# Optimization experiments

Hardware: AMD Instinct MI355X
Metric: run time of the kernel (lower is better)

The kernel has to match this reference:

```python
import jax, jax.numpy as jnp
import numpy as np

B, C, L = 4, 256, 2048
HEADS, DIM_HEAD = 8, 64
HIDDEN = HEADS * DIM_HEAD  # 512


def setup_inputs() -> dict:
    key = jax.random.key(0)
    k1, k2, k3, k4 = jax.random.split(key, 4)
    x = jax.random.normal(k1, (B, C, L), dtype=jnp.float32)
    # Conv1d kernel_size=1 weights, squeezed to [out_ch, in_ch]
    w_qkv = jax.random.normal(k2, (3 * HIDDEN, C), dtype=jnp.float32) * (1.0 / np.sqrt(C))
    w_out = jax.random.normal(k3, (C, HIDDEN), dtype=jnp.float32) * (1.0 / np.sqrt(HIDDEN))
    b_out = jax.random.normal(k4, (C,), dtype=jnp.float32) * 0.01
    return {"x": x, "w_qkv": w_qkv, "w_out": w_out, "b_out": b_out}


def reference(x, w_qkv, w_out, b_out):
    b, c, l = x.shape
    scale = DIM_HEAD ** (-0.5)
    # pointwise conv == channel matmul
    qkv = jnp.einsum('oc,bcl->bol', w_qkv, x)  # [b, 3*hidden, l]
    q, k, v = jnp.split(qkv, 3, axis=1)        # each [b, hidden, l]
    def to_heads(t):
        return t.reshape(b, HEADS, DIM_HEAD, l)  # b h d l
    q, k, v = to_heads(q), to_heads(k), to_heads(v)
    q = q * scale
    sim = jnp.einsum('bhdi,bhdj->bhij', q, k)   # [b,h,l,l]
    attn = jax.nn.softmax(sim, axis=-1)          # stable softmax (max-subtract inside)
    out = jnp.einsum('bhij,bhdj->bhid', attn, v)  # [b,h,l,d]
    out = out.transpose(0, 1, 3, 2).reshape(b, HIDDEN, l)  # b (h d) l
    return jnp.einsum('oc,bcl->bol', w_out, out) + b_out[None, :, None]
```

## Files before the change

### kernel.cpp

```cpp
#include <hip/hip_runtime.h>

typedef unsigned short u16;
typedef __bf16 bf16x8 __attribute__((ext_vector_type(8)));
typedef float f32x4 __attribute__((ext_vector_type(4)));

#define MFMA16(a, b, c) __builtin_amdgcn_mfma_f32_16x16x32_bf16((a), (b), (c), 0, 0, 0)

#define Bn 4
#define Cn 256
#define Ln 2048
#define Hn 8
#define Dn 64
#define HID 512

__device__ __forceinline__ u16 bf16_rne(float f) {
  unsigned u = __builtin_bit_cast(unsigned, f);
  u += 0x7FFFu + ((u >> 16) & 1u);
  return (u16)(u >> 16);
}

__device__ __forceinline__ float fast_exp2(float x) {
#if __has_builtin(__builtin_amdgcn_exp2f)
  return __builtin_amdgcn_exp2f(x);
#else
  return exp2f(x);
#endif
}

__device__ __forceinline__ float fast_rcp(float x) {
#if __has_builtin(__builtin_amdgcn_rcpf)
  return __builtin_amdgcn_rcpf(x);
#else
  return 1.0f / x;
#endif
}

__device__ __forceinline__ void async_load16(const u16* g, u16* l) {
  __builtin_amdgcn_global_load_lds(
      (const __attribute__((address_space(1))) void*)g,
      (__attribute__((address_space(3))) void*)l, 16, 0, 0);
}

__global__ __launch_bounds__(256) void prep_weights(const float* __restrict__ wqkv,
                                                    const float* __restrict__ wout,
                                                    u16* __restrict__ wq,
                                                    u16* __restrict__ wo) {
  int i = blockIdx.x * 256 + threadIdx.x;
  const float QSCALE = 0.125f * 1.44269504088896340736f;
  if (i < 3 * HID * Cn) {
    float v = wqkv[i];
    if (i < HID * Cn) v *= QSCALE;
    wq[i] = bf16_rne(v);
  } else {
    int j = i - 3 * HID * Cn;
    wo[j] = bf16_rne(wout[j]);
  }
}

__global__ __launch_bounds__(256) void transpose_x(const float* __restrict__ x,
                                                   u16* __restrict__ xT) {
  __shared__ u16 tile[64][72];
  const int b = blockIdx.z, ct = blockIdx.y, lt = blockIdx.x;
  const int t = threadIdx.x;
  const float* xp = x + ((size_t)b * Cn + ct * 64) * Ln + lt * 64;
  for (int pass = 0; pass < 4; ++pass) {
    int c = pass * 16 + (t >> 4);
    int l4 = (t & 15) * 4;
    float4 v = *(const float4*)(xp + (size_t)c * Ln + l4);
    tile[l4 + 0][c] = bf16_rne(v.x);
    tile[l4 + 1][c] = bf16_rne(v.y);
    tile[l4 + 2][c] = bf16_rne(v.z);
    tile[l4 + 3][c] = bf16_rne(v.w);
  }
  __syncthreads();
  u16* op = xT + ((size_t)b * Ln + lt * 64) * Cn + ct * 64;
  for (int pass = 0; pass < 2; ++pass) {
    int id = pass * 256 + t;
    int l = id >> 3, c8 = (id & 7) * 8;
    *(uint4*)(op + (size_t)l * Cn + c8) = *(const uint4*)&tile[l][c8];
  }
}

__global__ __launch_bounds__(256) void qkv_gemm(const u16* __restrict__ wq,
                                                const u16* __restrict__ xT,
                                                u16* __restrict__ qT,
                                                u16* __restrict__ kT,
                                                u16* __restrict__ vv) {
  __shared__ u16 As[4096];
  __shared__ u16 Bs[4096];
  const int t = threadIdx.x;
  const int nt = blockIdx.x, mt = blockIdx.y, b = blockIdx.z;
  const int m0 = mt * 64, n0 = nt * 64;
  const int w = t >> 6, lane = t & 63, q = lane >> 4, ln = lane & 15;

  const u16* Ag = wq + (size_t)m0 * Cn;
  const u16* Bg = xT + ((size_t)b * Ln + n0) * Cn;

  f32x4 zf = {0.f, 0.f, 0.f, 0.f};
  f32x4 acc[4];
  for (int i = 0; i < 4; ++i) acc[i] = zf;

  for (int kk = 0; kk < 4; ++kk) {
    int k0 = kk * 64;
    for (int k2 = 0; k2 < 2; ++k2) {
      int reg = k2 * 4 + w;
      int r = reg * 8 + (lane >> 3);
      int c = (lane & 7) ^ (r & 7);
      async_load16(Ag + (size_t)r * Cn + k0 + c * 8, &As[reg * 512]);
      async_load16(Bg + (size_t)r * Cn + k0 + c * 8, &Bs[reg * 512]);
    }
    __syncthreads();
    int ar = w * 16 + ln;
    bf16x8 a0 = *(const bf16x8*)&As[ar * 64 + ((q ^ (ln & 7)) * 8)];
    bf16x8 a1 = *(const bf16x8*)&As[ar * 64 + (((q + 4) ^ (ln & 7)) * 8)];
    for (int n2 = 0; n2 < 4; ++n2) {
      int br = n2 * 16 + ln;
      bf16x8 b0 = *(const bf16x8*)&Bs[br * 64 + ((q ^ (ln & 7)) * 8)];
      bf16x8 b1 = *(const bf16x8*)&Bs[br * 64 + (((q + 4) ^ (ln & 7)) * 8)];
      acc[n2] = MFMA16(a0, b0, acc[n2]);
      acc[n2] = MFMA16(a1, b1, acc[n2]);
    }
    __syncthreads();
  }
  for (int n2 = 0; n2 < 4; ++n2) {
    int l = n0 + n2 * 16 + ln;
    for (int r = 0; r < 4; ++r) {
      u16 hv = bf16_rne(acc[n2][r]);
      int od = w * 16 + q * 4 + r;
      if (mt < 8) {
        qT[(((size_t)b * Hn + mt) * Ln + l) * Dn + od] = hv;
      } else if (mt < 16) {
        kT[(((size_t)b * Hn + (mt - 8)) * Ln + l) * Dn + od] = hv;
      } else {
        int ch = (mt - 16) * 64 + od;
        vv[((size_t)b * HID + ch) * Ln + l] = hv;
      }
    }
  }
}

__global__ __launch_bounds__(256) void attention(const u16* __restrict__ qT,
                                                 const u16* __restrict__ kT,
                                                 const u16* __restrict__ vv,
                                                 u16* __restrict__ attT) {
  __shared__ u16 Kt[4096];
  __shared__ u16 Vt[4096];
  __shared__ u16 Ps[8192];
  const int t = threadIdx.x;
  const int qb = blockIdx.x, bh = blockIdx.y;
  const int b = bh >> 3, h = bh & 7;
  const int w = t >> 6, lane = t & 63, q = lane >> 4, ln = lane & 15;
  const int i0 = qb * 128 + w * 32;

  bf16x8 qa[2][2];
  for (int it = 0; it < 2; ++it) {
    const u16* qrow = qT + (((size_t)bh) * Ln + i0 + it * 16 + ln) * Dn;
    qa[it][0] = *(const bf16x8*)(qrow + q * 8);
    qa[it][1] = *(const bf16x8*)(qrow + 32 + q * 8);
  }

  const u16* ksrc0 = kT + ((size_t)bh) * Ln * Dn;
  const u16* vsrc0 = vv + ((size_t)b * HID + h * Dn) * Ln;

  bf16x8 ones;
  for (int i = 0; i < 8; ++i) ones[i] = (__bf16)1.0f;

  f32x4 zf = {0.f, 0.f, 0.f, 0.f};
  f32x4 o_acc[2][4], l_acc[2];
  for (int it = 0; it < 2; ++it) {
    l_acc[it] = zf;
    for (int d = 0; d < 4; ++d) o_acc[it][d] = zf;
  }
  u16* pw0 = Ps + w * 2048;

  for (int jt = 0; jt < 32; ++jt) {
    int j0 = jt * 64;
    for (int k2 = 0; k2 < 2; ++k2) {
      int reg = k2 * 4 + w;
      int r = reg * 8 + (lane >> 3);
      int c = (lane & 7) ^ (r & 7);
      async_load16(ksrc0 + (size_t)(j0 + r) * Dn + c * 8, &Kt[reg * 512]);
      async_load16(vsrc0 + (size_t)r * Ln + j0 + c * 8, &Vt[reg * 512]);
    }
    __syncthreads();

    f32x4 sv[2][4];
    for (int n2 = 0; n2 < 4; ++n2) {
      int jr = n2 * 16 + ln;
      bf16x8 k0f = *(const bf16x8*)&Kt[jr * 64 + ((q ^ (ln & 7)) * 8)];
      bf16x8 k1f = *(const bf16x8*)&Kt[jr * 64 + (((q + 4) ^ (ln & 7)) * 8)];
      for (int it = 0; it < 2; ++it) {
        f32x4 s = zf;
        s = MFMA16(k0f, qa[it][0], s);
        s = MFMA16(k1f, qa[it][1], s);
        sv[it][n2] = s;
      }
    }
    for (int it = 0; it < 2; ++it) {
      u16* pw = pw0 + it * 1024;
      for (int n2 = 0; n2 < 4; ++n2) {
        unsigned p01 = (unsigned)bf16_rne(fast_exp2(sv[it][n2][0])) |
                       ((unsigned)bf16_rne(fast_exp2(sv[it][n2][1])) << 16);
        unsigned p23 = (unsigned)bf16_rne(fast_exp2(sv[it][n2][2])) |
                       ((unsigned)bf16_rne(fast_exp2(sv[it][n2][3])) << 16);
        int jw = n2 * 16 + q * 4;
        int c = jw >> 3, lo = jw & 7;
        uint2 pk; pk.x = p01; pk.y = p23;
        *(uint2*)&pw[ln * 64 + ((c ^ (ln & 7)) * 8) + lo] = pk;
      }
    }
    for (int it = 0; it < 2; ++it) {
      u16* pw = pw0 + it * 1024;
      bf16x8 pa0 = *(const bf16x8*)&pw[ln * 64 + ((q ^ (ln & 7)) * 8)];
      bf16x8 pa1 = *(const bf16x8*)&pw[ln * 64 + (((q + 4) ^ (ln & 7)) * 8)];
      l_acc[it] = MFMA16(pa0, ones, l_acc[it]);
      l_acc[it] = MFMA16(pa1, ones, l_acc[it]);
      for (int d2 = 0; d2 < 4; ++d2) {
        int dr = d2 * 16 + ln;
        bf16x8 v0f = *(const bf16x8*)&Vt[dr * 64 + ((q ^ (ln & 7)) * 8)];
        bf16x8 v1f = *(const bf16x8*)&Vt[dr * 64 + (((q + 4) ^ (ln & 7)) * 8)];
        o_acc[it][d2] = MFMA16(pa0, v0f, o_acc[it][d2]);
        o_acc[it][d2] = MFMA16(pa1, v1f, o_acc[it][d2]);
      }
    }
    __syncthreads();
  }
  for (int it = 0; it < 2; ++it) {
    for (int r = 0; r < 4; ++r) {
      float rinv = fast_rcp(l_acc[it][r]);
      int i = i0 + it * 16 + q * 4 + r;
      size_t base = ((size_t)b * Ln + i) * HID + h * Dn;
      for (int d2 = 0; d2 < 4; ++d2)
        attT[base + d2 * 16 + ln] = bf16_rne(o_acc[it][d2][r] * rinv);
    }
  }
}

__global__ __launch_bounds__(256) void out_gemm(const u16* __restrict__ wo,
                                                const u16* __restrict__ attT,
                                                const float* __restrict__ bout,
                                                float* __restrict__ out) {
  __shared__ u16 As[4096];
  __shared__ u16 Bs[4096];
  const int t = threadIdx.x;
  const int nt = blockIdx.x, mt = blockIdx.y, b = blockIdx.z;
  const int m0 = mt * 64, n0 = nt * 64;
  const int w = t >> 6, lane = t & 63, q = lane >> 4, ln = lane & 15;

  const u16* Ag = wo + (size_t)m0 * HID;
  const u16* Bg = attT + ((size_t)b * Ln + n0) * HID;

  f32x4 zf = {0.f, 0.f, 0.f, 0.f};
  f32x4 acc[4];
  for (int i = 0; i < 4; ++i) acc[i] = zf;

  for (int kk = 0; kk < 8; ++kk) {
    int k0 = kk * 64;
    for (int k2 = 0; k2 < 2; ++k2) {
      int reg = k2 * 4 + w;
      int r = reg * 8 + (lane >> 3);
      int c = (lane & 7) ^ (r & 7);
      async_load16(Ag + (size_t)r * HID + k0 + c * 8, &As[reg * 512]);
      async_load16(Bg + (size_t)r * HID + k0 + c * 8, &Bs[reg * 512]);
    }
    __syncthreads();
    int ar = w * 16 + ln;
    bf16x8 a0 = *(const bf16x8*)&As[ar * 64 + ((q ^ (ln & 7)) * 8)];
    bf16x8 a1 = *(const bf16x8*)&As[ar * 64 + (((q + 4) ^ (ln & 7)) * 8)];
    for (int n2 = 0; n2 < 4; ++n2) {
      int br = n2 * 16 + ln;
      bf16x8 b0 = *(const bf16x8*)&Bs[br * 64 + ((q ^ (ln & 7)) * 8)];
      bf16x8 b1 = *(const bf16x8*)&Bs[br * 64 + (((q + 4) ^ (ln & 7)) * 8)];
      acc[n2] = MFMA16(a0, b0, acc[n2]);
      acc[n2] = MFMA16(a1, b1, acc[n2]);
    }
    __syncthreads();
  }
  float bias[4];
  for (int r = 0; r < 4; ++r) bias[r] = bout[m0 + w * 16 + q * 4 + r];
  for (int n2 = 0; n2 < 4; ++n2) {
    int l = n0 + n2 * 16 + ln;
    for (int r = 0; r < 4; ++r) {
      int o = m0 + w * 16 + q * 4 + r;
      out[((size_t)b * Cn + o) * Ln + l] = acc[n2][r] + bias[r];
    }
  }
}

extern "C" void kernel_launch(void* const* d_in, const int* in_sizes, int n_in,
                              void* d_out, int out_size, void* d_ws, size_t ws_size,
                              hipStream_t stream) {
  const float* x = (const float*)d_in[0];
  const float* wqkv = (const float*)d_in[1];
  const float* wout = (const float*)d_in[2];
  const float* bout = (const float*)d_in[3];
  float* out = (float*)d_out;
  char* ws = (char*)d_ws;

  u16* wq_b = (u16*)(ws + 0);
  u16* wo_b = (u16*)(ws + 786432);
  u16* xT   = (u16*)(ws + 1048576);
  u16* qT   = (u16*)(ws + 5242880);
  u16* kT   = (u16*)(ws + 13631488);
  u16* vv   = (u16*)(ws + 22020096);
  u16* attT = (u16*)(ws + 30408704);

  prep_weights<<<2048, 256, 0, stream>>>(wqkv, wout, wq_b, wo_b);
  transpose_x<<<dim3(32, 4, 4), 256, 0, stream>>>(x, xT);
  qkv_gemm<<<dim3(32, 24, 4), 256, 0, stream>>>(wq_b, xT, qT, kT, vv);
  attention<<<dim3(16, 32), 256, 0, stream>>>(qT, kT, vv, attT);
  out_gemm<<<dim3(32, 4, 4), 256, 0, stream>>>(wo_b, attT, bout, out);
}
```

Measured before the change: 168.9 us.

## Prefetch K/V tiles via registers and stage QKV epilogue through LDS

Measured after the change: 198.0 us. 1.17x slower.

```diff
diff --git a/kernel.cpp b/kernel.cpp
--- a/kernel.cpp
+++ b/kernel.cpp
@@ -17,6 +17,10 @@
   unsigned u = __builtin_bit_cast(unsigned, f);
   u += 0x7FFFu + ((u >> 16) & 1u);
   return (u16)(u >> 16);
+}
+
+__device__ __forceinline__ unsigned pack2(float a, float b) {
+  return (unsigned)bf16_rne(a) | ((unsigned)bf16_rne(b) << 16);
 }
 
 __device__ __forceinline__ float fast_exp2(float x) {
@@ -122,19 +126,42 @@
     }
     __syncthreads();
   }
-  for (int n2 = 0; n2 < 4; ++n2) {
-    int l = n0 + n2 * 16 + ln;
-    for (int r = 0; r < 4; ++r) {
-      u16 hv = bf16_rne(acc[n2][r]);
-      int od = w * 16 + q * 4 + r;
-      if (mt < 8) {
-        qT[(((size_t)b * Hn + mt) * Ln + l) * Dn + od] = hv;
-      } else if (mt < 16) {
-        kT[(((size_t)b * Hn + (mt - 8)) * Ln + l) * Dn + od] = hv;
-      } else {
-        int ch = (mt - 16) * 64 + od;
-        vv[((size_t)b * HID + ch) * Ln + l] = hv;
+
+  if (mt < 16) {
+    int od0 = w * 16 + q * 4;
+    int cw = od0 >> 3, lo = od0 & 7;
+    for (int n2 = 0; n2 < 4; ++n2) {
+      int l = n2 * 16 + ln;
+      uint2 pk;
+      pk.x = pack2(acc[n2][0], acc[n2][1]);
+      pk.y = pack2(acc[n2][2], acc[n2][3]);
+      *(uint2*)&As[l * 64 + ((cw ^ (l & 7)) * 8) + lo] = pk;
+    }
+    __syncthreads();
+    u16* dst = (mt < 8) ? qT + (((size_t)b * Hn + mt) * Ln + n0) * Dn
+                        : kT + (((size_t)b * Hn + (mt - 8)) * Ln + n0) * Dn;
+    for (int pass = 0; pass < 2; ++pass) {
+      int id = pass * 256 + t;
+      int l = id >> 3, c = id & 7;
+      *(uint4*)(dst + (size_t)l * Dn + c * 8) =
+          *(const uint4*)&As[l * 64 + ((c ^ (l & 7)) * 8)];
+    }
+  } else {
+    for (int n2 = 0; n2 < 4; ++n2) {
+      int l = n2 * 16 + ln;
+      int cl = l >> 3, lo = l & 7;
+      for (int r = 0; r < 4; ++r) {
+        int od = w * 16 + q * 4 + r;
+        As[od * 64 + ((cl ^ (od & 7)) * 8) + lo] = bf16_rne(acc[n2][r]);
       }
+    }
+    __syncthreads();
+    u16* dst = vv + ((size_t)b * HID + (mt - 16) * 64) * Ln + n0;
+    for (int pass = 0; pass < 2; ++pass) {
+      int id = pass * 256 + t;
+      int od = id >> 3, c = id & 7;
+      *(uint4*)(dst + (size_t)od * Ln + c * 8) =
+          *(const uint4*)&As[od * 64 + ((c ^ (od & 7)) * 8)];
     }
   }
 }
@@ -173,17 +200,24 @@
   }
   u16* pw0 = Ps + w * 2048;
 
-  for (int jt = 0; jt < 32; ++jt) {
+  const int pr0 = w * 8 + (lane >> 3), pr1 = (4 + w) * 8 + (lane >> 3);
+  const int pc0 = (lane & 7) ^ (pr0 & 7), pc1 = (lane & 7) ^ (pr1 & 7);
+
+  auto loadKV = [&](int jt, uint4* kr, uint4* vr) {
     int j0 = jt * 64;
-    for (int k2 = 0; k2 < 2; ++k2) {
-      int reg = k2 * 4 + w;
-      int r = reg * 8 + (lane >> 3);
-      int c = (lane & 7) ^ (r & 7);
-      async_load16(ksrc0 + (size_t)(j0 + r) * Dn + c * 8, &Kt[reg * 512]);
-      async_load16(vsrc0 + (size_t)r * Ln + j0 + c * 8, &Vt[reg * 512]);
-    }
-    __syncthreads();
-
+    kr[0] = *(const uint4*)(ksrc0 + (size_t)(j0 + pr0) * Dn + pc0 * 8);
+    kr[1] = *(const uint4*)(ksrc0 + (size_t)(j0 + pr1) * Dn + pc1 * 8);
+    vr[0] = *(const uint4*)(vsrc0 + (size_t)pr0 * Ln + j0 + pc0 * 8);
+    vr[1] = *(const uint4*)(vsrc0 + (size_t)pr1 * Ln + j0 + pc1 * 8);
+  };
+  auto storeKV = [&](const uint4* kr, const uint4* vr) {
+    *(uint4*)&Kt[w * 512 + lane * 8] = kr[0];
+    *(uint4*)&Kt[(4 + w) * 512 + lane * 8] = kr[1];
+    *(uint4*)&Vt[w * 512 + lane * 8] = vr[0];
+    *(uint4*)&Vt[(4 + w) * 512 + lane * 8] = vr[1];
+  };
+
+  auto compute = [&]() {
     f32x4 sv[2][4];
     for (int n2 = 0; n2 < 4; ++n2) {
       int jr = n2 * 16 + ln;
@@ -199,13 +233,11 @@
     for (int it = 0; it < 2; ++it) {
       u16* pw = pw0 + it * 1024;
       for (int n2 = 0; n2 < 4; ++n2) {
-        unsigned p01 = (unsigned)bf16_rne(fast_exp2(sv[it][n2][0])) |
-                       ((unsigned)bf16_rne(fast_exp2(sv[it][n2][1])) << 16);
-        unsigned p23 = (unsigned)bf16_rne(fast_exp2(sv[it][n2][2])) |
-                       ((unsigned)bf16_rne(fast_exp2(sv[it][n2][3])) << 16);
+        uint2 pk;
+        pk.x = pack2(fast_exp2(sv[it][n2][0]), fast_exp2(sv[it][n2][1]));
+        pk.y = pack2(fast_exp2(sv[it][n2][2]), fast_exp2(sv[it][n2][3]));
         int jw = n2 * 16 + q * 4;
         int c = jw >> 3, lo = jw & 7;
-        uint2 pk; pk.x = p01; pk.y = p23;
         *(uint2*)&pw[ln * 64 + ((c ^ (ln & 7)) * 8) + lo] = pk;
       }
     }
@@ -223,8 +255,23 @@
         o_acc[it][d2] = MFMA16(pa1, v1f, o_acc[it][d2]);
       }
     }
-    __syncthreads();
-  }
+  };
+
+  uint4 ka[2], va[2], kb[2], vb[2];
+  loadKV(0, ka, va);
+  for (int jt = 0; jt < 32; jt += 2) {
+    if (jt) __syncthreads();
+    storeKV(ka, va);
+    __syncthreads();
+    loadKV(jt + 1, kb, vb);
+    compute();
+    __syncthreads();
+    storeKV(kb, vb);
+    __syncthreads();
+    if (jt + 2 < 32) loadKV(jt + 2, ka, va);
+    compute();
+  }
+
   for (int it = 0; it < 2; ++it) {
     for (int r = 0; r < 4; ++r) {
       float rinv = fast_rcp(l_acc[it][r]);
@@ -254,16 +301,23 @@
   f32x4 acc[4];
   for (int i = 0; i < 4; ++i) acc[i] = zf;
 
-  for (int kk = 0; kk < 8; ++kk) {
+  const int pr0 = w * 8 + (lane >> 3), pr1 = (4 + w) * 8 + (lane >> 3);
+  const int pc0 = (lane & 7) ^ (pr0 & 7), pc1 = (lane & 7) ^ (pr1 & 7);
+
+  auto loadAB = [&](int kk, uint4* ar, uint4* br) {
     int k0 = kk * 64;
-    for (int k2 = 0; k2 < 2; ++k2) {
-      int reg = k2 * 4 + w;
-      int r = reg * 8 + (lane >> 3);
-      int c = (lane & 7) ^ (r & 7);
-      async_load16(Ag + (size_t)r * HID + k0 + c * 8, &As[reg * 512]);
-      async_load16(Bg + (size_t)r * HID + k0 + c * 8, &Bs[reg * 512]);
-    }
-    __syncthreads();
+    ar[0] = *(const uint4*)(Ag + (size_t)pr0 * HID + k0 + pc0 * 8);
+    ar[1] = *(const uint4*)(Ag + (size_t)pr1 * HID + k0 + pc1 * 8);
+    br[0] = *(const uint4*)(Bg + (size_t)pr0 * HID + k0 + pc0 * 8);
+    br[1] = *(const uint4*)(Bg + (size_t)pr1 * HID + k0 + pc1 * 8);
+  };
+  auto storeAB = [&](const uint4* ar, const uint4* br) {
+    *(uint4*)&As[w * 512 + lane * 8] = ar[0];
+    *(uint4*)&As[(4 + w) * 512 + lane * 8] = ar[1];
+    *(uint4*)&Bs[w * 512 + lane * 8] = br[0];
+    *(uint4*)&Bs[(4 + w) * 512 + lane * 8] = br[1];
+  };
+  auto computeC = [&]() {
     int ar = w * 16 + ln;
     bf16x8 a0 = *(const bf16x8*)&As[ar * 64 + ((q ^ (ln & 7)) * 8)];
     bf16x8 a1 = *(const bf16x8*)&As[ar * 64 + (((q + 4) ^ (ln & 7)) * 8)];
@@ -274,8 +328,23 @@
       acc[n2] = MFMA16(a0, b0, acc[n2]);
       acc[n2] = MFMA16(a1, b1, acc[n2]);
     }
-    __syncthreads();
-  }
+  };
+
+  uint4 aa[2], ba[2], ab[2], bb[2];
+  loadAB(0, aa, ba);
+  for (int kk = 0; kk < 8; kk += 2) {
+    if (kk) __syncthreads();
+    storeAB(aa, ba);
+    __syncthreads();
+    loadAB(kk + 1, ab, bb);
+    computeC();
+    __syncthreads();
+    storeAB(ab, bb);
+    __syncthreads();
+    if (kk + 2 < 8) loadAB(kk + 2, aa, ba);
+    computeC();
+  }
+
   float bias[4];
   for (int r = 0; r < 4; ++r) bias[r] = bout[m0 + w * 16 + q * 4 + r];
   for (int n2 = 0; n2 < 4; ++n2) {
```
